# Kernel tuning notes

Hardware: AMD Instinct MI355X
Metric: run time of the kernel (lower is better)

Reference implementation:

```python
import jax, jax.numpy as jnp
import numpy as np

L = 16                                 # n_levels
T = 1 << 19                            # 2^log2_hashmap_size entries per level
BASE = 16.0                            # base_resolution
PLS = float(np.exp(np.log(4096.0 / 16.0) / (L - 1)))  # per_level_scale
PRIMES = (1, 2654435761, 805459861)    # instant-ngp spatial hash primes


def _hashgrid_encode(x, grid):
    """x: [N,3] in [0,1]; grid: [L,T,2]. Returns [N, L*2] trilinear hash-grid features."""
    feats = []
    for l in range(L):
        scale = BASE * (PLS ** l) - 1.0
        res = int(np.ceil(scale)) + 1
        pos = x * scale + 0.5
        p0f = jnp.floor(pos)
        frac = pos - p0f                       # [N,3]
        p0 = p0f.astype(jnp.uint32)
        dense = (res ** 3) <= T                # low-res levels indexed densely
        f = jnp.zeros((x.shape[0], 2), dtype=grid.dtype)
        for c in range(8):                     # 8 trilinear corners
            off = np.array([(c >> d) & 1 for d in range(3)], dtype=np.uint32)
            pc = p0 + off                      # [N,3] uint32
            if dense:
                pc = jnp.minimum(pc, np.uint32(res - 1))
                idx = pc[:, 0] + pc[:, 1] * np.uint32(res) + pc[:, 2] * np.uint32(res * res)
            else:
                h = ((pc[:, 0] * np.uint32(PRIMES[0]))
                     ^ (pc[:, 1] * np.uint32(PRIMES[1]))
                     ^ (pc[:, 2] * np.uint32(PRIMES[2])))
                idx = h & np.uint32(T - 1)
            w = jnp.prod(jnp.where(off == 1, frac, 1.0 - frac), axis=-1)  # [N]
            f = f + w[:, None] * grid[l, idx]
        feats.append(f)
    return jnp.concatenate(feats, axis=-1)     # [N, 32]


def setup_inputs() -> dict:
    key = jax.random.key(0)
    ks = jax.random.split(key, 6)
    N = 4_194_304
    texc = jax.random.uniform(ks[0], (N, 3), jnp.float32, -1.2, 1.2)
    grid = jax.random.uniform(ks[1], (L, T, 2), jnp.float32, -1e-4, 1e-4)
    s = np.float32(np.sqrt(2.0 / 32.0))        # kaiming-uniform scale-ish
    W0 = jax.random.normal(ks[2], (32, 32), jnp.float32) * s
    W1 = jax.random.normal(ks[3], (32, 32), jnp.float32) * s
    W2 = jax.random.normal(ks[4], (9, 32), jnp.float32) * s
    AABB = jnp.array([[-1.0, -1.0, -1.0], [1.0, 1.0, 1.0]], jnp.float32)
    min_max = jnp.stack([jnp.zeros(9, jnp.float32), jnp.ones(9, jnp.float32)])
    return {"texc": texc, "grid": grid, "W0": W0, "W1": W1, "W2": W2,
            "AABB": AABB, "min_max": min_max}


def reference(texc, grid, W0, W1, W2, AABB, min_max):
    u = jnp.clip((texc - AABB[0]) / (AABB[1] - AABB[0]), 0.0, 1.0)  # [N,3]
    enc = _hashgrid_encode(u, grid)                                  # [N,32]
    h = jax.nn.relu(enc @ W0.T)
    h = jax.nn.relu(h @ W1.T)
    out = h @ W2.T                                                   # [N,9]
    return jax.nn.sigmoid(out) * (min_max[1] - min_max[0]) + min_max[0]
```

## Files before the change

kernel.cpp:

```cpp
#include <hip/hip_runtime.h>
#include <hip/hip_fp16.h>
#include <stdint.h>

#define TSIZE (1u << 19)
#define NLEV 16

__device__ constexpr float SC[NLEV] = {
    15.0f,          22.1563078f,   32.5134119f,   47.5029301f,
    69.1967987f,    100.5936673f,  146.0333894f,  211.7969328f,
    306.9744096f,   444.7218880f,  644.0795776f,  932.6038304f,
    1350.1761008f,  1954.5156576f, 2829.1576190f, 4095.0f};
__device__ constexpr uint32_t RES[5] = {16u, 24u, 34u, 49u, 71u};

static __device__ __forceinline__ uint32_t umin32(uint32_t a, uint32_t b) {
    return a < b ? a : b;
}

static __device__ __forceinline__ void level_idx(int l, float ux, float uy, float uz,
                                                 uint32_t* idxs) {
    const float s = SC[l];
    float px = fmaf(ux, s, 0.5f);
    float py = fmaf(uy, s, 0.5f);
    float pz = fmaf(uz, s, 0.5f);
    uint32_t x0 = (uint32_t)floorf(px);
    uint32_t y0 = (uint32_t)floorf(py);
    uint32_t z0 = (uint32_t)floorf(pz);
    if (l < 5) {
        const uint32_t R = RES[l];
        uint32_t xs[2] = {umin32(x0, R - 1u), umin32(x0 + 1u, R - 1u)};
        uint32_t ys[2] = {umin32(y0, R - 1u), umin32(y0 + 1u, R - 1u)};
        uint32_t zs[2] = {umin32(z0, R - 1u), umin32(z0 + 1u, R - 1u)};
#pragma unroll
        for (int c = 0; c < 8; ++c)
            idxs[c] = xs[c & 1] + ys[(c >> 1) & 1] * R + zs[c >> 2] * R * R;
    } else {
        uint32_t hx[2] = {x0, x0 + 1u};
        uint32_t hy0 = y0 * 2654435761u;
        uint32_t hz0 = z0 * 805459861u;
        uint32_t hy[2] = {hy0, hy0 + 2654435761u};
        uint32_t hz[2] = {hz0, hz0 + 805459861u};
#pragma unroll
        for (int c = 0; c < 8; ++c)
            idxs[c] = (hx[c & 1] ^ hy[(c >> 1) & 1] ^ hz[c >> 2]) & (TSIZE - 1u);
    }
}

__global__ __launch_bounds__(256) void convert_grid(const float2* __restrict__ g,
                                                    __half2* __restrict__ o, int n) {
    int i = blockIdx.x * 256 + threadIdx.x;
    if (i < n) {
        float2 v = g[i];
        o[i] = __floats2half2_rn(v.x, v.y);
    }
}

__global__ __launch_bounds__(256) void mlp_tex3d_h(
    const float* __restrict__ texc,
    const __half2* __restrict__ gws,
    const float* __restrict__ W0,
    const float* __restrict__ W1,
    const float* __restrict__ W2,
    const float* __restrict__ aabb,
    const float* __restrict__ mm,
    float* __restrict__ out,
    int N)
{
    int i = blockIdx.x * 256 + threadIdx.x;
    if (i >= N) return;

    float t0 = texc[3 * i + 0], t1 = texc[3 * i + 1], t2 = texc[3 * i + 2];
    float ux = fminf(fmaxf((t0 - aabb[0]) / (aabb[3] - aabb[0]), 0.f), 1.f);
    float uy = fminf(fmaxf((t1 - aabb[1]) / (aabb[4] - aabb[1]), 0.f), 1.f);
    float uz = fminf(fmaxf((t2 - aabb[2]) / (aabb[5] - aabb[2]), 0.f), 1.f);

    __half2 gb[4][8];
#pragma unroll
    for (int l = 0; l < 4; ++l) {
        uint32_t idxs[8];
        level_idx(l, ux, uy, uz, idxs);
        const __half2* __restrict__ gl = gws + (size_t)l * TSIZE;
#pragma unroll
        for (int c = 0; c < 8; ++c) gb[l][c] = gl[idxs[c]];
    }

    float enc[32];
#pragma unroll
    for (int l = 0; l < NLEV; ++l) {
        const float s = SC[l];
        float px = fmaf(ux, s, 0.5f);
        float py = fmaf(uy, s, 0.5f);
        float pz = fmaf(uz, s, 0.5f);
        float rx = px - floorf(px), ry = py - floorf(py), rz = pz - floorf(pz);
        float wx[2] = {1.f - rx, rx};
        float wy[2] = {1.f - ry, ry};
        float wz[2] = {1.f - rz, rz};
        float f0 = 0.f, f1 = 0.f;
#pragma unroll
        for (int c = 0; c < 8; ++c) {
            float2 g = __half22float2(gb[l & 3][c]);
            float w = wx[c & 1] * wy[(c >> 1) & 1] * wz[c >> 2];
            f0 = fmaf(w, g.x, f0);
            f1 = fmaf(w, g.y, f1);
        }
        enc[2 * l + 0] = f0;
        enc[2 * l + 1] = f1;
        if (l + 4 < NLEV) {
            uint32_t idxs[8];
            level_idx(l + 4, ux, uy, uz, idxs);
            const __half2* __restrict__ gl = gws + (size_t)(l + 4) * TSIZE;
#pragma unroll
            for (int c = 0; c < 8; ++c) gb[(l + 4) & 3][c] = gl[idxs[c]];
        }
    }

    float h[32];
#pragma unroll
    for (int j = 0; j < 32; ++j) {
        float a = 0.f;
#pragma unroll
        for (int k = 0; k < 32; ++k) a = fmaf(enc[k], W0[j * 32 + k], a);
        h[j] = fmaxf(a, 0.f);
    }
#pragma unroll
    for (int j = 0; j < 32; ++j) {
        float a = 0.f;
#pragma unroll
        for (int k = 0; k < 32; ++k) a = fmaf(h[k], W1[j * 32 + k], a);
        enc[j] = fmaxf(a, 0.f);
    }
#pragma unroll
    for (int j = 0; j < 9; ++j) {
        float a = 0.f;
#pragma unroll
        for (int k = 0; k < 32; ++k) a = fmaf(enc[k], W2[j * 32 + k], a);
        float sg = 1.0f / (1.0f + __expf(-a));
        out[(size_t)i * 9 + j] = fmaf(sg, mm[9 + j] - mm[j], mm[j]);
    }
}

__global__ __launch_bounds__(256) void mlp_tex3d_f(
    const float* __restrict__ texc, const float2* __restrict__ grid,
    const float* __restrict__ W0, const float* __restrict__ W1,
    const float* __restrict__ W2, const float* __restrict__ aabb,
    const float* __restrict__ mm, float* __restrict__ out, int N)
{
    int i = blockIdx.x * 256 + threadIdx.x;
    if (i >= N) return;
    float t0 = texc[3 * i + 0], t1 = texc[3 * i + 1], t2 = texc[3 * i + 2];
    float ux = fminf(fmaxf((t0 - aabb[0]) / (aabb[3] - aabb[0]), 0.f), 1.f);
    float uy = fminf(fmaxf((t1 - aabb[1]) / (aabb[4] - aabb[1]), 0.f), 1.f);
    float uz = fminf(fmaxf((t2 - aabb[2]) / (aabb[5] - aabb[2]), 0.f), 1.f);
    float enc[32];
#pragma unroll
    for (int l = 0; l < NLEV; ++l) {
        const float s = SC[l];
        float px = fmaf(ux, s, 0.5f), py = fmaf(uy, s, 0.5f), pz = fmaf(uz, s, 0.5f);
        float rx = px - floorf(px), ry = py - floorf(py), rz = pz - floorf(pz);
        float wx[2] = {1.f - rx, rx}, wy[2] = {1.f - ry, ry}, wz[2] = {1.f - rz, rz};
        uint32_t idxs[8];
        level_idx(l, ux, uy, uz, idxs);
        const float2* __restrict__ gl = grid + (size_t)l * TSIZE;
        float f0 = 0.f, f1 = 0.f;
#pragma unroll
        for (int c = 0; c < 8; ++c) {
            float2 g = gl[idxs[c]];
            float w = wx[c & 1] * wy[(c >> 1) & 1] * wz[c >> 2];
            f0 = fmaf(w, g.x, f0);
            f1 = fmaf(w, g.y, f1);
        }
        enc[2 * l + 0] = f0;
        enc[2 * l + 1] = f1;
    }
    float h[32];
#pragma unroll
    for (int j = 0; j < 32; ++j) {
        float a = 0.f;
#pragma unroll
        for (int k = 0; k < 32; ++k) a = fmaf(enc[k], W0[j * 32 + k], a);
        h[j] = fmaxf(a, 0.f);
    }
#pragma unroll
    for (int j = 0; j < 32; ++j) {
        float a = 0.f;
#pragma unroll
        for (int k = 0; k < 32; ++k) a = fmaf(h[k], W1[j * 32 + k], a);
        enc[j] = fmaxf(a, 0.f);
    }
#pragma unroll
    for (int j = 0; j < 9; ++j) {
        float a = 0.f;
#pragma unroll
        for (int k = 0; k < 32; ++k) a = fmaf(enc[k], W2[j * 32 + k], a);
        float sg = 1.0f / (1.0f + __expf(-a));
        out[(size_t)i * 9 + j] = fmaf(sg, mm[9 + j] - mm[j], mm[j]);
    }
}

extern "C" void kernel_launch(void* const* d_in, const int* in_sizes, int n_in,
                              void* d_out, int out_size, void* d_ws, size_t ws_size,
                              hipStream_t stream) {
    const float*  texc = (const float*)d_in[0];
    const float2* grid = (const float2*)d_in[1];
    const float*  W0   = (const float*)d_in[2];
    const float*  W1   = (const float*)d_in[3];
    const float*  W2   = (const float*)d_in[4];
    const float*  aabb = (const float*)d_in[5];
    const float*  mm   = (const float*)d_in[6];
    float* out = (float*)d_out;

    int N = in_sizes[0] / 3;
    int blocks = (N + 255) / 256;
    const int ngrid = NLEV * TSIZE;
    const size_t need = (size_t)ngrid * sizeof(__half2);

    if (ws_size >= need) {
        __half2* gws = (__half2*)d_ws;
        convert_grid<<<(ngrid + 255) / 256, 256, 0, stream>>>(grid, gws, ngrid);
        mlp_tex3d_h<<<blocks, 256, 0, stream>>>(texc, gws, W0, W1, W2, aabb, mm, out, N);
    } else {
        mlp_tex3d_f<<<blocks, 256, 0, stream>>>(texc, grid, W0, W1, W2, aabb, mm, out, N);
    }
}
```

Before: 2.371 ms.

## Prefetch all hash-level gathers upfront and fuse first MLP layer into encoding

Issues all 88 hash-level grid gathers (11 levels x 8 corners) at kernel start, behind a scheduling barrier, so their latency overlaps with the dense-level gathers and compute. The first linear layer is fused into the per-level interpolation, accumulating h directly instead of building the full 32-wide encoding first. Launch bounds now request 3 blocks per CU. Holding 88 half2 values in registers raises VGPR pressure and may cause spills or lower occupancy, in exchange for more memory-level parallelism.

```diff
diff --git a/kernel.cpp b/kernel.cpp
--- a/kernel.cpp
+++ b/kernel.cpp
@@ -4,45 +4,61 @@
 
 #define TSIZE (1u << 19)
 #define NLEV 16
+#define NDENSE 5
+#define NHASH (NLEV - NDENSE)
 
 __device__ constexpr float SC[NLEV] = {
     15.0f,          22.1563078f,   32.5134119f,   47.5029301f,
     69.1967987f,    100.5936673f,  146.0333894f,  211.7969328f,
     306.9744096f,   444.7218880f,  644.0795776f,  932.6038304f,
     1350.1761008f,  1954.5156576f, 2829.1576190f, 4095.0f};
-__device__ constexpr uint32_t RES[5] = {16u, 24u, 34u, 49u, 71u};
+__device__ constexpr uint32_t RES[NDENSE] = {16u, 24u, 34u, 49u, 71u};
 
 static __device__ __forceinline__ uint32_t umin32(uint32_t a, uint32_t b) {
     return a < b ? a : b;
 }
 
-static __device__ __forceinline__ void level_idx(int l, float ux, float uy, float uz,
+static __device__ __forceinline__ void hash_idx(int l, float ux, float uy, float uz,
+                                                uint32_t* idxs) {
+    const float s = SC[l];
+    uint32_t x0 = (uint32_t)floorf(fmaf(ux, s, 0.5f));
+    uint32_t y0 = (uint32_t)floorf(fmaf(uy, s, 0.5f));
+    uint32_t z0 = (uint32_t)floorf(fmaf(uz, s, 0.5f));
+    uint32_t hy0 = y0 * 2654435761u;
+    uint32_t hz0 = z0 * 805459861u;
+    uint32_t hx[2] = {x0, x0 + 1u};
+    uint32_t hy[2] = {hy0, hy0 + 2654435761u};
+    uint32_t hz[2] = {hz0, hz0 + 805459861u};
+#pragma unroll
+    for (int c = 0; c < 8; ++c)
+        idxs[c] = (hx[c & 1] ^ hy[(c >> 1) & 1] ^ hz[c >> 2]) & (TSIZE - 1u);
+}
+
+static __device__ __forceinline__ void dense_idx(int l, float ux, float uy, float uz,
                                                  uint32_t* idxs) {
+    const float s = SC[l];
+    const uint32_t R = RES[l];
+    uint32_t x0 = (uint32_t)floorf(fmaf(ux, s, 0.5f));
+    uint32_t y0 = (uint32_t)floorf(fmaf(uy, s, 0.5f));
+    uint32_t z0 = (uint32_t)floorf(fmaf(uz, s, 0.5f));
+    uint32_t xs[2] = {umin32(x0, R - 1u), umin32(x0 + 1u, R - 1u)};
+    uint32_t ys[2] = {umin32(y0, R - 1u), umin32(y0 + 1u, R - 1u)};
+    uint32_t zs[2] = {umin32(z0, R - 1u), umin32(z0 + 1u, R - 1u)};
+#pragma unroll
+    for (int c = 0; c < 8; ++c)
+        idxs[c] = xs[c & 1] + ys[(c >> 1) & 1] * R + zs[c >> 2] * R * R;
+}
+
+static __device__ __forceinline__ void level_w(int l, float ux, float uy, float uz,
+                                               float* wx, float* wy, float* wz) {
     const float s = SC[l];
     float px = fmaf(ux, s, 0.5f);
     float py = fmaf(uy, s, 0.5f);
     float pz = fmaf(uz, s, 0.5f);
-    uint32_t x0 = (uint32_t)floorf(px);
-    uint32_t y0 = (uint32_t)floorf(py);
-    uint32_t z0 = (uint32_t)floorf(pz);
-    if (l < 5) {
-        const uint32_t R = RES[l];
-        uint32_t xs[2] = {umin32(x0, R - 1u), umin32(x0 + 1u, R - 1u)};
-        uint32_t ys[2] = {umin32(y0, R - 1u), umin32(y0 + 1u, R - 1u)};
-        uint32_t zs[2] = {umin32(z0, R - 1u), umin32(z0 + 1u, R - 1u)};
-#pragma unroll
-        for (int c = 0; c < 8; ++c)
-            idxs[c] = xs[c & 1] + ys[(c >> 1) & 1] * R + zs[c >> 2] * R * R;
-    } else {
-        uint32_t hx[2] = {x0, x0 + 1u};
-        uint32_t hy0 = y0 * 2654435761u;
-        uint32_t hz0 = z0 * 805459861u;
-        uint32_t hy[2] = {hy0, hy0 + 2654435761u};
-        uint32_t hz[2] = {hz0, hz0 + 805459861u};
-#pragma unroll
-        for (int c = 0; c < 8; ++c)
-            idxs[c] = (hx[c & 1] ^ hy[(c >> 1) & 1] ^ hz[c >> 2]) & (TSIZE - 1u);
-    }
+    float rx = px - floorf(px), ry = py - floorf(py), rz = pz - floorf(pz);
+    wx[0] = 1.f - rx; wx[1] = rx;
+    wy[0] = 1.f - ry; wy[1] = ry;
+    wz[0] = 1.f - rz; wz[1] = rz;
 }
 
 __global__ __launch_bounds__(256) void convert_grid(const float2* __restrict__ g,
@@ -54,7 +70,7 @@
     }
 }
 
-__global__ __launch_bounds__(256) void mlp_tex3d_h(
+__global__ __launch_bounds__(256, 3) void mlp_tex3d_h(
     const float* __restrict__ texc,
     const __half2* __restrict__ gws,
     const float* __restrict__ W0,
@@ -73,66 +89,77 @@
     float uy = fminf(fmaxf((t1 - aabb[1]) / (aabb[4] - aabb[1]), 0.f), 1.f);
     float uz = fminf(fmaxf((t2 - aabb[2]) / (aabb[5] - aabb[2]), 0.f), 1.f);
 
-    __half2 gb[4][8];
-#pragma unroll
-    for (int l = 0; l < 4; ++l) {
+    __half2 gb[NHASH][8];
+#pragma unroll
+    for (int l = NDENSE; l < NLEV; ++l) {
         uint32_t idxs[8];
-        level_idx(l, ux, uy, uz, idxs);
+        hash_idx(l, ux, uy, uz, idxs);
         const __half2* __restrict__ gl = gws + (size_t)l * TSIZE;
 #pragma unroll
-        for (int c = 0; c < 8; ++c) gb[l][c] = gl[idxs[c]];
-    }
-
-    float enc[32];
-#pragma unroll
-    for (int l = 0; l < NLEV; ++l) {
-        const float s = SC[l];
-        float px = fmaf(ux, s, 0.5f);
-        float py = fmaf(uy, s, 0.5f);
-        float pz = fmaf(uz, s, 0.5f);
-        float rx = px - floorf(px), ry = py - floorf(py), rz = pz - floorf(pz);
-        float wx[2] = {1.f - rx, rx};
-        float wy[2] = {1.f - ry, ry};
-        float wz[2] = {1.f - rz, rz};
+        for (int c = 0; c < 8; ++c) gb[l - NDENSE][c] = gl[idxs[c]];
+    }
+    __builtin_amdgcn_sched_barrier(0);
+
+    float h[32];
+#pragma unroll
+    for (int j = 0; j < 32; ++j) h[j] = 0.f;
+
+#pragma unroll
+    for (int l = 0; l < NDENSE; ++l) {
+        uint32_t idxs[8];
+        dense_idx(l, ux, uy, uz, idxs);
+        const __half2* __restrict__ gl = gws + (size_t)l * TSIZE;
+        float wx[2], wy[2], wz[2];
+        level_w(l, ux, uy, uz, wx, wy, wz);
         float f0 = 0.f, f1 = 0.f;
 #pragma unroll
         for (int c = 0; c < 8; ++c) {
-            float2 g = __half22float2(gb[l & 3][c]);
+            float2 g = __half22float2(gl[idxs[c]]);
             float w = wx[c & 1] * wy[(c >> 1) & 1] * wz[c >> 2];
             f0 = fmaf(w, g.x, f0);
             f1 = fmaf(w, g.y, f1);
         }
-        enc[2 * l + 0] = f0;
-        enc[2 * l + 1] = f1;
-        if (l + 4 < NLEV) {
-            uint32_t idxs[8];
-            level_idx(l + 4, ux, uy, uz, idxs);
-            const __half2* __restrict__ gl = gws + (size_t)(l + 4) * TSIZE;
-#pragma unroll
-            for (int c = 0; c < 8; ++c) gb[(l + 4) & 3][c] = gl[idxs[c]];
-        }
-    }
-
-    float h[32];
+#pragma unroll
+        for (int j = 0; j < 32; ++j) {
+            h[j] = fmaf(f0, W0[j * 32 + 2 * l], h[j]);
+            h[j] = fmaf(f1, W0[j * 32 + 2 * l + 1], h[j]);
+        }
+    }
+
+#pragma unroll
+    for (int l = NDENSE; l < NLEV; ++l) {
+        float wx[2], wy[2], wz[2];
+        level_w(l, ux, uy, uz, wx, wy, wz);
+        float f0 = 0.f, f1 = 0.f;
+#pragma unroll
+        for (int c = 0; c < 8; ++c) {
+            float2 g = __half22float2(gb[l - NDENSE][c]);
+            float w = wx[c & 1] * wy[(c >> 1) & 1] * wz[c >> 2];
+            f0 = fmaf(w, g.x, f0);
+            f1 = fmaf(w, g.y, f1);
+        }
+#pragma unroll
+        for (int j = 0; j < 32; ++j) {
+            h[j] = fmaf(f0, W0[j * 32 + 2 * l], h[j]);
+            h[j] = fmaf(f1, W0[j * 32 + 2 * l + 1], h[j]);
+        }
+    }
+
+    float h2[32];
+#pragma unroll
+    for (int j = 0; j < 32; ++j) h[j] = fmaxf(h[j], 0.f);
 #pragma unroll
     for (int j = 0; j < 32; ++j) {
         float a = 0.f;
 #pragma unroll
-        for (int k = 0; k < 32; ++k) a = fmaf(enc[k], W0[j * 32 + k], a);
-        h[j] = fmaxf(a, 0.f);
-    }
-#pragma unroll
-    for (int j = 0; j < 32; ++j) {
-        float a = 0.f;
-#pragma unroll
         for (int k = 0; k < 32; ++k) a = fmaf(h[k], W1[j * 32 + k], a);
-        enc[j] = fmaxf(a, 0.f);
+        h2[j] = fmaxf(a, 0.f);
     }
 #pragma unroll
     for (int j = 0; j < 9; ++j) {
         float a = 0.f;
 #pragma unroll
-        for (int k = 0; k < 32; ++k) a = fmaf(enc[k], W2[j * 32 + k], a);
+        for (int k = 0; k < 32; ++k) a = fmaf(h2[k], W2[j * 32 + k], a);
         float sg = 1.0f / (1.0f + __expf(-a));
         out[(size_t)i * 9 + j] = fmaf(sg, mm[9 + j] - mm[j], mm[j]);
     }
@@ -153,12 +180,11 @@
     float enc[32];
 #pragma unroll
     for (int l = 0; l < NLEV; ++l) {
-        const float s = SC[l];
-        float px = fmaf(ux, s, 0.5f), py = fmaf(uy, s, 0.5f), pz = fmaf(uz, s, 0.5f);
-        float rx = px - floorf(px), ry = py - floorf(py), rz = pz - floorf(pz);
-        float wx[2] = {1.f - rx, rx}, wy[2] = {1.f - ry, ry}, wz[2] = {1.f - rz, rz};
         uint32_t idxs[8];
-        level_idx(l, ux, uy, uz, idxs);
+        if (l < NDENSE) dense_idx(l, ux, uy, uz, idxs);
+        else            hash_idx(l, ux, uy, uz, idxs);
+        float wx[2], wy[2], wz[2];
+        level_w(l, ux, uy, uz, wx, wy, wz);
         const float2* __restrict__ gl = grid + (size_t)l * TSIZE;
         float f0 = 0.f, f1 = 0.f;
 #pragma unroll
```

Result: slower. 2.698 ms (+13.8%).
